# Optimization experiments

Hardware: AMD Instinct MI355X
Metric: run time of the kernel (lower is better)

The kernel has to match this reference:

```python
import jax, jax.numpy as jnp
import numpy as np
from jax import lax

B, T, C = 256, 128, 512
HID, HOR = 1024, 96
THR = 1.0


def setup_inputs() -> dict:
    key = jax.random.key(0)
    ks = jax.random.split(key, 6)
    x = jax.random.normal(ks[0], (B, T, C), dtype=jnp.float32)
    # fc1: Linear(C -> HID), PyTorch layout [out, in]
    W1 = jax.random.normal(ks[1], (HID, C), dtype=jnp.float32) / np.sqrt(C)
    b1 = jax.random.normal(ks[2], (HID,), dtype=jnp.float32) * 0.01
    # head: Linear(HID -> HOR)
    Wh = jax.random.normal(ks[3], (HOR, HID), dtype=jnp.float32) / np.sqrt(HID)
    bh = jax.random.normal(ks[4], (HOR,), dtype=jnp.float32) * 0.01
    beta = jnp.float32(0.9)  # learnable leak (snntorch Leaky, learn_beta=True)
    return {"x": x, "W1": W1, "b1": b1, "Wh": Wh, "bh": bh, "beta": beta}


def reference(x, W1, b1, Wh, bh, beta):
    # Precompute all fc1 projections as one batched GEMM: [B,T,HID]
    proj = jnp.einsum("btc,hc->bth", x, W1) + b1
    beta_c = jnp.clip(beta, 0.0, 1.0)

    def step(mem, inp):
        # snntorch Leaky, reset_mechanism='subtract': reset based on PREVIOUS mem
        reset = (mem > THR).astype(mem.dtype)  # detached in snntorch
        mem_new = beta_c * mem + inp - reset * THR
        return mem_new, None

    mem0 = jnp.zeros((x.shape[0], W1.shape[0]), dtype=x.dtype)
    mem_T, _ = lax.scan(step, mem0, jnp.moveaxis(proj, 1, 0))  # scan over T
    return mem_T @ Wh.T + bh  # [B, HOR]
```

## Files before the change

### kernel.cpp

```cpp
#include <hip/hip_runtime.h>

#define TT 128
#define CC 512
#define HIDN 1024
#define HORN 96
#define NB 256
#define BM 128
#define BN 128
#define BK 64
#define NSTAGE 8

typedef _Float16 f16x8 __attribute__((ext_vector_type(8)));
typedef _Float16 f16x4 __attribute__((ext_vector_type(4)));
typedef float f32x16 __attribute__((ext_vector_type(16)));

#define XHI 0
#define XLO 16384
#define WHI 32768
#define WLO 49152
#define SMEM_BYTES 67584

__device__ __forceinline__ void cvt_split(const float4 v, f16x4* hi, f16x4* lo) {
    auto h01 = __builtin_amdgcn_cvt_pkrtz(v.x, v.y);
    auto h23 = __builtin_amdgcn_cvt_pkrtz(v.z, v.w);
    auto l01 = __builtin_amdgcn_cvt_pkrtz(v.x - (float)h01.x, v.y - (float)h01.y);
    auto l23 = __builtin_amdgcn_cvt_pkrtz(v.z - (float)h23.x, v.w - (float)h23.y);
    *hi = (f16x4){(_Float16)h01.x, (_Float16)h01.y, (_Float16)h23.x, (_Float16)h23.y};
    *lo = (f16x4){(_Float16)l01.x, (_Float16)l01.y, (_Float16)l23.x, (_Float16)l23.y};
}

__global__ void __launch_bounds__(256, 2)
snn_proj_scan(const float* __restrict__ x, const float* __restrict__ W1,
              const float* __restrict__ b1, const float* __restrict__ betap,
              float* __restrict__ memT)
{
    __shared__ __align__(16) char smem[SMEM_BYTES];

    const int tid  = threadIdx.x;
    const int lane = tid & 63;
    const int wid  = tid >> 6;
    const int wm = wid >> 1, wn = wid & 1;
    const int g2 = lane >> 5, lr = lane & 31;

    const int lid  = blockIdx.x;
    const int slot = lid >> 3;
    const int b     = ((lid & 7) << 5) + (slot >> 3);
    const int hbase = (slot & 7) * BN;

    const float* __restrict__ xg = x  + (size_t)b * TT * CC;
    const float* __restrict__ wg = W1 + (size_t)hbase * CC;

    const int srow = tid >> 4;
    const int skq  = tid & 15;
    const float* xrow = xg + srow * CC + skq * 4;
    const float* wrow = wg + srow * CC + skq * 4;
    const int wbyte = (skq * 8) ^ ((srow & 7) << 4);

    const int sw    = (lr & 7) << 4;
    const int arow0 = (wm * 64 +  0 + lr) * 128;
    const int arow1 = (wm * 64 + 32 + lr) * 128;
    const int brow0 = (wn * 64 +  0 + lr) * 128;
    const int brow1 = (wn * 64 + 32 + lr) * 128;

    f32x16 acc00 = {}, acc01 = {}, acc10 = {}, acc11 = {};

    float4 px[8], pw[8];
#pragma unroll
    for (int p = 0; p < 8; ++p) {
        px[p] = *(const float4*)(xrow + p * 16 * CC);
        pw[p] = *(const float4*)(wrow + p * 16 * CC);
    }

    for (int s = 0; s < NSTAGE; ++s) {
#pragma unroll
        for (int p = 0; p < 8; ++p) {
            const int byte = (srow + 16 * p) * 128 + wbyte;
            f16x4 hi, lo;
            cvt_split(px[p], &hi, &lo);
            *(f16x4*)(smem + XHI + byte) = hi;
            *(f16x4*)(smem + XLO + byte) = lo;
            cvt_split(pw[p], &hi, &lo);
            *(f16x4*)(smem + WHI + byte) = hi;
            *(f16x4*)(smem + WLO + byte) = lo;
        }
        __syncthreads();

        if (s + 1 < NSTAGE) {
            const int ko = (s + 1) * BK;
#pragma unroll
            for (int p = 0; p < 8; ++p) {
                px[p] = *(const float4*)(xrow + p * 16 * CC + ko);
                pw[p] = *(const float4*)(wrow + p * 16 * CC + ko);
            }
        }

#pragma unroll
        for (int ks = 0; ks < 4; ++ks) {
            const int off = ((ks << 5) | (g2 << 4)) ^ sw;
            const f16x8 ah0 = *(const f16x8*)(smem + XHI + arow0 + off);
            const f16x8 ah1 = *(const f16x8*)(smem + XHI + arow1 + off);
            const f16x8 al0 = *(const f16x8*)(smem + XLO + arow0 + off);
            const f16x8 al1 = *(const f16x8*)(smem + XLO + arow1 + off);
            const f16x8 bh0 = *(const f16x8*)(smem + WHI + brow0 + off);
            const f16x8 bh1 = *(const f16x8*)(smem + WHI + brow1 + off);
            const f16x8 bl0 = *(const f16x8*)(smem + WLO + brow0 + off);
            const f16x8 bl1 = *(const f16x8*)(smem + WLO + brow1 + off);

            acc00 = __builtin_amdgcn_mfma_f32_32x32x16_f16(ah0, bh0, acc00, 0, 0, 0);
            acc00 = __builtin_amdgcn_mfma_f32_32x32x16_f16(ah0, bl0, acc00, 0, 0, 0);
            acc00 = __builtin_amdgcn_mfma_f32_32x32x16_f16(al0, bh0, acc00, 0, 0, 0);

            acc01 = __builtin_amdgcn_mfma_f32_32x32x16_f16(ah0, bh1, acc01, 0, 0, 0);
            acc01 = __builtin_amdgcn_mfma_f32_32x32x16_f16(ah0, bl1, acc01, 0, 0, 0);
            acc01 = __builtin_amdgcn_mfma_f32_32x32x16_f16(al0, bh1, acc01, 0, 0, 0);

            acc10 = __builtin_amdgcn_mfma_f32_32x32x16_f16(ah1, bh0, acc10, 0, 0, 0);
            acc10 = __builtin_amdgcn_mfma_f32_32x32x16_f16(ah1, bl0, acc10, 0, 0, 0);
            acc10 = __builtin_amdgcn_mfma_f32_32x32x16_f16(al1, bh0, acc10, 0, 0, 0);

            acc11 = __builtin_amdgcn_mfma_f32_32x32x16_f16(ah1, bh1, acc11, 0, 0, 0);
            acc11 = __builtin_amdgcn_mfma_f32_32x32x16_f16(ah1, bl1, acc11, 0, 0, 0);
            acc11 = __builtin_amdgcn_mfma_f32_32x32x16_f16(al1, bh1, acc11, 0, 0, 0);
        }
        __syncthreads();
    }

#define ST_ACC(A, m, n) {                                                        \
        char* rp = smem + (wn * 64 + (n) * 32 + lr) * 528                        \
                        + (wm * 64 + (m) * 32 + 4 * g2) * 4;                     \
        *(float4*)(rp +  0) = make_float4(A[0],  A[1],  A[2],  A[3]);            \
        *(float4*)(rp + 32) = make_float4(A[4],  A[5],  A[6],  A[7]);            \
        *(float4*)(rp + 64) = make_float4(A[8],  A[9],  A[10], A[11]);           \
        *(float4*)(rp + 96) = make_float4(A[12], A[13], A[14], A[15]); }
    ST_ACC(acc00, 0, 0)
    ST_ACC(acc01, 0, 1)
    ST_ACC(acc10, 1, 0)
    ST_ACC(acc11, 1, 1)
#undef ST_ACC
    __syncthreads();

    if (tid < BN) {
        const float beta_c = fminf(fmaxf(betap[0], 0.0f), 1.0f);
        const float b1h = b1[hbase + tid];
        const char* rp = smem + tid * 528;
        float mem = 0.0f;
#pragma unroll
        for (int q = 0; q < 32; ++q) {
            const float4 v = *(const float4*)(rp + 16 * q);
            float reset;
            reset = (mem > 1.0f) ? 1.0f : 0.0f; mem = beta_c * mem + (v.x + b1h) - reset;
            reset = (mem > 1.0f) ? 1.0f : 0.0f; mem = beta_c * mem + (v.y + b1h) - reset;
            reset = (mem > 1.0f) ? 1.0f : 0.0f; mem = beta_c * mem + (v.z + b1h) - reset;
            reset = (mem > 1.0f) ? 1.0f : 0.0f; mem = beta_c * mem + (v.w + b1h) - reset;
        }
        memT[(size_t)b * HIDN + hbase + tid] = mem;
    }
}

__global__ void __launch_bounds__(192)
snn_head(const float* __restrict__ memT, const float* __restrict__ Wh,
         const float* __restrict__ bh, float* __restrict__ out)
{
    __shared__ __align__(16) float ms[4 * HIDN];
    const int tid = threadIdx.x;
    const int bbase = blockIdx.x * 4;
    const float4* src = (const float4*)(memT + (size_t)bbase * HIDN);
    for (int i = tid; i < HIDN; i += 192)
        ((float4*)ms)[i] = src[i];
    __syncthreads();

    const int o = tid % 96, grp = tid / 96;
    const float4* wr = (const float4*)(Wh + (size_t)o * HIDN);
    const float4* m0 = (const float4*)(ms + (grp * 2 + 0) * HIDN);
    const float4* m1 = (const float4*)(ms + (grp * 2 + 1) * HIDN);
    float a0 = 0.f, a1 = 0.f;
    for (int q = 0; q < HIDN / 4; ++q) {
        const float4 w = wr[q];
        const float4 u = m0[q];
        const float4 v = m1[q];
        a0 = fmaf(w.x, u.x, fmaf(w.y, u.y, fmaf(w.z, u.z, fmaf(w.w, u.w, a0))));
        a1 = fmaf(w.x, v.x, fmaf(w.y, v.y, fmaf(w.z, v.z, fmaf(w.w, v.w, a1))));
    }
    const float bo = bh[o];
    out[(size_t)(bbase + grp * 2 + 0) * HORN + o] = a0 + bo;
    out[(size_t)(bbase + grp * 2 + 1) * HORN + o] = a1 + bo;
}

extern "C" void kernel_launch(void* const* d_in, const int* in_sizes, int n_in,
                              void* d_out, int out_size, void* d_ws, size_t ws_size,
                              hipStream_t stream)
{
    (void)in_sizes; (void)n_in; (void)out_size; (void)ws_size;
    const float* x    = (const float*)d_in[0];
    const float* W1   = (const float*)d_in[1];
    const float* b1   = (const float*)d_in[2];
    const float* Wh   = (const float*)d_in[3];
    const float* bh   = (const float*)d_in[4];
    const float* beta = (const float*)d_in[5];

    float* memT = (float*)d_ws;

    snn_proj_scan<<<2048, 256, 0, stream>>>(x, W1, b1, beta, memT);
    snn_head<<<64, 192, 0, stream>>>(memT, Wh, bh, (float*)d_out);
}
```

Before: 237.5 us.

## Preconvert W1 to fp16 hi/lo once and stream it into LDS directly

A new pre-pass kernel splits W1 into fp16 hi/lo halves once per call. The main kernel then loads those halves straight into LDS with global_load_lds, which removes the per-block fp32 weight loads and repeated conversions from registers. The accumulator staging buffer switches from a padded row layout to an XOR-swizzled one so shared memory drops to 64KB. The head kernel is rewritten to use one block per batch row with a wave-level shuffle reduction. The cost is an extra kernel launch and a W1 round trip through the workspace.

```diff
diff --git a/kernel.cpp b/kernel.cpp
--- a/kernel.cpp
+++ b/kernel.cpp
@@ -5,7 +5,6 @@
 #define HIDN 1024
 #define HORN 96
 #define NB 256
-#define BM 128
 #define BN 128
 #define BK 64
 #define NSTAGE 8
@@ -18,7 +17,7 @@
 #define XLO 16384
 #define WHI 32768
 #define WLO 49152
-#define SMEM_BYTES 67584
+#define SMEM_BYTES 65536
 
 __device__ __forceinline__ void cvt_split(const float4 v, f16x4* hi, f16x4* lo) {
     auto h01 = __builtin_amdgcn_cvt_pkrtz(v.x, v.y);
@@ -29,10 +28,27 @@
     *lo = (f16x4){(_Float16)l01.x, (_Float16)l01.y, (_Float16)l23.x, (_Float16)l23.y};
 }
 
+__device__ __forceinline__ void gload16(const void* g, void* l) {
+    __builtin_amdgcn_global_load_lds(
+        (const __attribute__((address_space(1))) unsigned int*)g,
+        (__attribute__((address_space(3))) unsigned int*)l, 16, 0, 0);
+}
+
+__global__ void __launch_bounds__(256)
+snn_cvtw(const float* __restrict__ W1, f16x4* __restrict__ whi, f16x4* __restrict__ wlo)
+{
+    const int i = blockIdx.x * 256 + threadIdx.x;
+    const float4 v = ((const float4*)W1)[i];
+    f16x4 hi, lo;
+    cvt_split(v, &hi, &lo);
+    whi[i] = hi;
+    wlo[i] = lo;
+}
+
 __global__ void __launch_bounds__(256, 2)
-snn_proj_scan(const float* __restrict__ x, const float* __restrict__ W1,
-              const float* __restrict__ b1, const float* __restrict__ betap,
-              float* __restrict__ memT)
+snn_proj_scan(const float* __restrict__ x, const _Float16* __restrict__ whi_g,
+              const _Float16* __restrict__ wlo_g, const float* __restrict__ b1,
+              const float* __restrict__ betap, float* __restrict__ memT)
 {
     __shared__ __align__(16) char smem[SMEM_BYTES];
 
@@ -47,14 +63,17 @@
     const int b     = ((lid & 7) << 5) + (slot >> 3);
     const int hbase = (slot & 7) * BN;
 
-    const float* __restrict__ xg = x  + (size_t)b * TT * CC;
-    const float* __restrict__ wg = W1 + (size_t)hbase * CC;
+    const float* __restrict__ xg = x + (size_t)b * TT * CC;
 
     const int srow = tid >> 4;
     const int skq  = tid & 15;
     const float* xrow = xg + srow * CC + skq * 4;
-    const float* wrow = wg + srow * CC + skq * 4;
     const int wbyte = (skq * 8) ^ ((srow & 7) << 4);
+
+    const int wrow0  = lane >> 3;
+    const int wslotb = ((lane & 7) ^ wrow0) * 16;
+    const char* whsrc = (const char*)whi_g + ((size_t)(hbase + wrow0) * CC) * 2 + wslotb;
+    const char* wlsrc = (const char*)wlo_g + ((size_t)(hbase + wrow0) * CC) * 2 + wslotb;
 
     const int sw    = (lr & 7) << 4;
     const int arow0 = (wm * 64 +  0 + lr) * 128;
@@ -64,14 +83,18 @@
 
     f32x16 acc00 = {}, acc01 = {}, acc10 = {}, acc11 = {};
 
-    float4 px[8], pw[8];
-#pragma unroll
-    for (int p = 0; p < 8; ++p) {
-        px[p] = *(const float4*)(xrow + p * 16 * CC);
-        pw[p] = *(const float4*)(wrow + p * 16 * CC);
-    }
+    float4 px[8];
+#pragma unroll
+    for (int p = 0; p < 8; ++p) px[p] = *(const float4*)(xrow + p * 16 * CC);
 
     for (int s = 0; s < NSTAGE; ++s) {
+#pragma unroll
+        for (int c = 0; c < 4; ++c) {
+            const int chunk = wid * 4 + c;
+            const size_t go = (size_t)chunk * (8 * CC * 2) + (size_t)s * (BK * 2);
+            gload16(whsrc + go, smem + WHI + chunk * 1024);
+            gload16(wlsrc + go, smem + WLO + chunk * 1024);
+        }
 #pragma unroll
         for (int p = 0; p < 8; ++p) {
             const int byte = (srow + 16 * p) * 128 + wbyte;
@@ -79,19 +102,14 @@
             cvt_split(px[p], &hi, &lo);
             *(f16x4*)(smem + XHI + byte) = hi;
             *(f16x4*)(smem + XLO + byte) = lo;
-            cvt_split(pw[p], &hi, &lo);
-            *(f16x4*)(smem + WHI + byte) = hi;
-            *(f16x4*)(smem + WLO + byte) = lo;
         }
         __syncthreads();
 
         if (s + 1 < NSTAGE) {
             const int ko = (s + 1) * BK;
 #pragma unroll
-            for (int p = 0; p < 8; ++p) {
+            for (int p = 0; p < 8; ++p)
                 px[p] = *(const float4*)(xrow + p * 16 * CC + ko);
-                pw[p] = *(const float4*)(wrow + p * 16 * CC + ko);
-            }
         }
 
 #pragma unroll
@@ -126,12 +144,14 @@
     }
 
 #define ST_ACC(A, m, n) {                                                        \
-        char* rp = smem + (wn * 64 + (n) * 32 + lr) * 528                        \
-                        + (wm * 64 + (m) * 32 + 4 * g2) * 4;                     \
-        *(float4*)(rp +  0) = make_float4(A[0],  A[1],  A[2],  A[3]);            \
-        *(float4*)(rp + 32) = make_float4(A[4],  A[5],  A[6],  A[7]);            \
-        *(float4*)(rp + 64) = make_float4(A[8],  A[9],  A[10], A[11]);           \
-        *(float4*)(rp + 96) = make_float4(A[12], A[13], A[14], A[15]); }
+        const int row   = wn * 64 + (n) * 32 + lr;                               \
+        const int sbase = wm * 16 + (m) * 8 + g2;                                \
+        const int rs    = row & 31;                                              \
+        char* rb = smem + row * 512;                                             \
+        *(float4*)(rb + (((sbase + 0) ^ rs) * 16)) = make_float4(A[0],  A[1],  A[2],  A[3]);  \
+        *(float4*)(rb + (((sbase + 2) ^ rs) * 16)) = make_float4(A[4],  A[5],  A[6],  A[7]);  \
+        *(float4*)(rb + (((sbase + 4) ^ rs) * 16)) = make_float4(A[8],  A[9],  A[10], A[11]); \
+        *(float4*)(rb + (((sbase + 6) ^ rs) * 16)) = make_float4(A[12], A[13], A[14], A[15]); }
     ST_ACC(acc00, 0, 0)
     ST_ACC(acc01, 0, 1)
     ST_ACC(acc10, 1, 0)
@@ -142,11 +162,12 @@
     if (tid < BN) {
         const float beta_c = fminf(fmaxf(betap[0], 0.0f), 1.0f);
         const float b1h = b1[hbase + tid];
-        const char* rp = smem + tid * 528;
+        const char* rb = smem + tid * 512;
+        const int rs = tid & 31;
         float mem = 0.0f;
 #pragma unroll
         for (int q = 0; q < 32; ++q) {
-            const float4 v = *(const float4*)(rp + 16 * q);
+            const float4 v = *(const float4*)(rb + ((q ^ rs) * 16));
             float reset;
             reset = (mem > 1.0f) ? 1.0f : 0.0f; mem = beta_c * mem + (v.x + b1h) - reset;
             reset = (mem > 1.0f) ? 1.0f : 0.0f; mem = beta_c * mem + (v.y + b1h) - reset;
@@ -157,33 +178,30 @@
     }
 }
 
-__global__ void __launch_bounds__(192)
+__global__ void __launch_bounds__(256)
 snn_head(const float* __restrict__ memT, const float* __restrict__ Wh,
          const float* __restrict__ bh, float* __restrict__ out)
 {
-    __shared__ __align__(16) float ms[4 * HIDN];
+    __shared__ __align__(16) float ms[HIDN];
+    const int b   = blockIdx.x;
     const int tid = threadIdx.x;
-    const int bbase = blockIdx.x * 4;
-    const float4* src = (const float4*)(memT + (size_t)bbase * HIDN);
-    for (int i = tid; i < HIDN; i += 192)
-        ((float4*)ms)[i] = src[i];
+    ((float4*)ms)[tid] = ((const float4*)(memT + (size_t)b * HIDN))[tid];
     __syncthreads();
 
-    const int o = tid % 96, grp = tid / 96;
-    const float4* wr = (const float4*)(Wh + (size_t)o * HIDN);
-    const float4* m0 = (const float4*)(ms + (grp * 2 + 0) * HIDN);
-    const float4* m1 = (const float4*)(ms + (grp * 2 + 1) * HIDN);
-    float a0 = 0.f, a1 = 0.f;
-    for (int q = 0; q < HIDN / 4; ++q) {
-        const float4 w = wr[q];
-        const float4 u = m0[q];
-        const float4 v = m1[q];
-        a0 = fmaf(w.x, u.x, fmaf(w.y, u.y, fmaf(w.z, u.z, fmaf(w.w, u.w, a0))));
-        a1 = fmaf(w.x, v.x, fmaf(w.y, v.y, fmaf(w.z, v.z, fmaf(w.w, v.w, a1))));
+    const int lane = tid & 63, wid = tid >> 6;
+    for (int o = wid; o < HORN; o += 4) {
+        const float4* wr = (const float4*)(Wh + (size_t)o * HIDN);
+        float a = 0.0f;
+#pragma unroll
+        for (int q = 0; q < 4; ++q) {
+            const float4 w = wr[q * 64 + lane];
+            const float4 m = ((const float4*)ms)[q * 64 + lane];
+            a = fmaf(w.x, m.x, fmaf(w.y, m.y, fmaf(w.z, m.z, fmaf(w.w, m.w, a))));
+        }
+#pragma unroll
+        for (int d = 32; d; d >>= 1) a += __shfl_xor(a, d);
+        if (lane == 0) out[(size_t)b * HORN + o] = a + bh[o];
     }
-    const float bo = bh[o];
-    out[(size_t)(bbase + grp * 2 + 0) * HORN + o] = a0 + bo;
-    out[(size_t)(bbase + grp * 2 + 1) * HORN + o] = a1 + bo;
 }
 
 extern "C" void kernel_launch(void* const* d_in, const int* in_sizes, int n_in,
@@ -198,8 +216,12 @@
     const float* bh   = (const float*)d_in[4];
     const float* beta = (const float*)d_in[5];
 
-    float* memT = (float*)d_ws;
-
-    snn_proj_scan<<<2048, 256, 0, stream>>>(x, W1, b1, beta, memT);
-    snn_head<<<64, 192, 0, stream>>>(memT, Wh, bh, (float*)d_out);
-}
+    char* ws = (char*)d_ws;
+    _Float16* whi = (_Float16*)(ws);
+    _Float16* wlo = (_Float16*)(ws + (1 << 20));
+    float*    memT = (float*)(ws + (2 << 20));
+
+    snn_cvtw<<<512, 256, 0, stream>>>(W1, (f16x4*)whi, (f16x4*)wlo);
+    snn_proj_scan<<<2048, 256, 0, stream>>>(x, whi, wlo, b1, beta, memT);
+    snn_head<<<NB, 256, 0, stream>>>(memT, Wh, bh, (float*)d_out);
+}
```

Result: faster. 213.2 us (-10.2%).
